# Optimization experiments

Hardware: AMD Instinct MI355X
Metric: run time of the kernel (lower is better)

The kernel has to match this reference:

```python
import jax, jax.numpy as jnp
import numpy as np

NETS = 32
NODES = [256, 512, 512, 128]
BATCH = 4096


def setup_inputs() -> dict:
    key = jax.random.key(0)
    ks = jax.random.split(key, 7)
    def lin_init(k, n_out, n_in):
        # mimic nn.Linear default init scale
        bound = 1.0 / np.sqrt(n_in)
        kw, kb = jax.random.split(k)
        W = jax.random.uniform(kw, (NETS, n_out, n_in), jnp.float32, -bound, bound)
        b = jax.random.uniform(kb, (NETS, n_out), jnp.float32, -bound, bound)
        return W, b
    x = jax.random.normal(ks[0], (BATCH, NODES[0]), jnp.float32)
    W1, b1 = lin_init(ks[1], NODES[1], NODES[0])
    W2, b2 = lin_init(ks[2], NODES[2], NODES[1])
    W3, b3 = lin_init(ks[3], NODES[3], NODES[2])
    return {"x": x, "W1": W1, "b1": b1, "W2": W2, "b2": b2, "W3": W3, "b3": b3}


def reference(x, W1, b1, W2, b2, W3, b3):
    # Ensemble of independent MLPs expressed as batched GEMMs over the `nets` axis.
    # x: [B, in]; Wl: [N, out_l, in_l]; bl: [N, out_l]
    h = jax.nn.relu(jnp.einsum('bi,noi->bno', x, W1) + b1)        # [B, N, 512]
    h = jax.nn.relu(jnp.einsum('bni,noi->bno', h, W2) + b2)       # [B, N, 512]
    out = jnp.einsum('bni,noi->bno', h, W3) + b3                  # [B, N, 128] (identity act)
    B = x.shape[0]
    # Concatenate per-net outputs along feature dim: y[:, n*out_len:(n+1)*out_len]
    return out.reshape(B, -1)
```

## Files before the change

### kernel.cpp

```cpp
#include <hip/hip_runtime.h>

#define NETS 32
#define BATCH 4096
#define D0 256
#define D1 512
#define D2 512
#define D3 128
#define MT 64
#define LDA (D0 + 8)
#define LDH (D1 + 8)

using half8 = __attribute__((ext_vector_type(8))) _Float16;
using half4 = __attribute__((ext_vector_type(4))) _Float16;
using f32x4 = __attribute__((ext_vector_type(4))) float;

#define W1_N (NETS * D1 * D0)
#define W2_N (NETS * D2 * D1)
#define W3_N (NETS * D3 * D2)

__global__ void cvt_weights(const float* __restrict__ W1, const float* __restrict__ W2,
                            const float* __restrict__ W3,
                            _Float16* __restrict__ W1h, _Float16* __restrict__ W2h,
                            _Float16* __restrict__ W3h) {
    const int i = blockIdx.x * blockDim.x + threadIdx.x;
    constexpr int T1 = W1_N / 8, T2 = W2_N / 8, T3 = W3_N / 8;
    const float* src;
    _Float16* dst;
    if (i < T1) {
        int u = i, l = u & 63, f = u >> 6;
        int kkni = f & 63, netw = f >> 6;
        int ni = kkni & 7, kk = kkni >> 3;
        int net = netw >> 2, w = netw & 3;
        int n = w * 128 + ni * 16 + (l & 15);
        int k = kk * 32 + (l >> 4) * 8;
        src = W1 + (size_t)net * D1 * D0 + (size_t)n * D0 + k;
        dst = W1h + (size_t)f * 512 + l * 8;
    } else if (i < T1 + T2) {
        int u = i - T1, l = u & 63, f = u >> 6;
        int kkni = f & 127, netw = f >> 7;
        int ni = kkni & 7, kk = kkni >> 3;
        int net = netw >> 2, w = netw & 3;
        int n = w * 128 + ni * 16 + (l & 15);
        int k = kk * 32 + (l >> 4) * 8;
        src = W2 + (size_t)net * D2 * D1 + (size_t)n * D1 + k;
        dst = W2h + (size_t)f * 512 + l * 8;
    } else {
        int u = i - T1 - T2, l = u & 63, f = u >> 6;
        int kkni = f & 31, netw = f >> 5;
        int ni = kkni & 1, kk = kkni >> 1;
        int net = netw >> 2, w = netw & 3;
        int n = w * 32 + ni * 16 + (l & 15);
        int k = kk * 32 + (l >> 4) * 8;
        src = W3 + (size_t)net * D3 * D2 + (size_t)n * D2 + k;
        dst = W3h + (size_t)f * 512 + l * 8;
    }
    float4 v0 = *reinterpret_cast<const float4*>(src);
    float4 v1 = *reinterpret_cast<const float4*>(src + 4);
    half8 o;
    o[0] = (_Float16)v0.x; o[1] = (_Float16)v0.y; o[2] = (_Float16)v0.z; o[3] = (_Float16)v0.w;
    o[4] = (_Float16)v1.x; o[5] = (_Float16)v1.y; o[6] = (_Float16)v1.z; o[7] = (_Float16)v1.w;
    *reinterpret_cast<half8*>(dst) = o;
}

template<int K, int NI, int G, int MI>
__device__ __forceinline__ void layer_mfma(const _Float16* As, int lda,
                                           const _Float16* __restrict__ wl,
                                           int lane16, int quad,
                                           f32x4 (&acc)[MI][NI]) {
    constexpr int NFR = (K / 32) * NI;
    constexpr int STEPS = NFR / G;
    half8 bcur[G], bnxt[G];
    half8 a[MI];
#pragma unroll
    for (int g = 0; g < G; ++g)
        bcur[g] = *reinterpret_cast<const half8*>(wl + (size_t)g * 512);
#pragma unroll
    for (int s = 0; s < STEPS; ++s) {
        const int fb = s * G;
        if (s + 1 < STEPS) {
#pragma unroll
            for (int g = 0; g < G; ++g)
                bnxt[g] = *reinterpret_cast<const half8*>(wl + (size_t)(fb + G + g) * 512);
        }
        if (fb % NI == 0) {
            const int kk = fb / NI;
#pragma unroll
            for (int mi = 0; mi < MI; ++mi)
                a[mi] = *reinterpret_cast<const half8*>(
                    As + (mi * 16 + lane16) * lda + kk * 32 + quad * 8);
        }
#pragma unroll
        for (int g = 0; g < G; ++g) {
            const int ni = (fb + g) % NI;
#pragma unroll
            for (int mi = 0; mi < MI; ++mi)
                acc[mi][ni] = __builtin_amdgcn_mfma_f32_16x16x32_f16(a[mi], bcur[g], acc[mi][ni], 0, 0, 0);
        }
        if (s + 1 < STEPS) {
#pragma unroll
            for (int g = 0; g < G; ++g) bcur[g] = bnxt[g];
        }
    }
}

template<int MI, int NI>
__device__ __forceinline__ void store_act(f32x4 (&acc)[MI][NI], const float* __restrict__ bias,
                                          _Float16* dst, int ldd, int n_base,
                                          int lane16, int quad) {
#pragma unroll
    for (int ni = 0; ni < NI; ++ni) {
        float bv = bias[n_base + ni * 16 + lane16];
        int col = n_base + ni * 16 + lane16;
#pragma unroll
        for (int mi = 0; mi < MI; ++mi) {
#pragma unroll
            for (int r = 0; r < 4; ++r) {
                float v = acc[mi][ni][r] + bv;
                v = fmaxf(v, 0.0f);
                int row = mi * 16 + quad * 4 + r;
                dst[row * ldd + col] = (_Float16)v;
            }
        }
    }
}

__global__ __launch_bounds__(256, 2) void mlp_fused(
    const float* __restrict__ X,
    const _Float16* __restrict__ W1h, const float* __restrict__ b1,
    const _Float16* __restrict__ W2h, const float* __restrict__ b2,
    const _Float16* __restrict__ W3h, const float* __restrict__ b3,
    float* __restrict__ out) {
    __shared__ __align__(16) _Float16 buf[MT * LDH];

    const int tid = threadIdx.x;
    const int w = tid >> 6;
    const int l = tid & 63;
    const int lane16 = l & 15;
    const int quad = l >> 4;

    const int bb = blockIdx.x;
    const int xcd = bb & 7;
    const int s = bb >> 3;
    const int net = xcd * 4 + (s >> 6);
    const int mt = s & 63;
    const int m0 = mt * MT;

    {
        const float* xsrc = X + (size_t)m0 * D0;
#pragma unroll
        for (int it = 0; it < 16; ++it) {
            int chunk = it * 256 + tid;
            int row = chunk >> 6;
            int c4 = chunk & 63;
            float4 v = *reinterpret_cast<const float4*>(xsrc + row * D0 + c4 * 4);
            half4 o;
            o[0] = (_Float16)v.x; o[1] = (_Float16)v.y;
            o[2] = (_Float16)v.z; o[3] = (_Float16)v.w;
            *reinterpret_cast<half4*>(&buf[row * LDA + c4 * 4]) = o;
        }
    }
    __syncthreads();

    {
        f32x4 acc[4][8] = {};
        const _Float16* wl = W1h + ((size_t)(net * 4 + w) * 64) * 512 + l * 8;
        layer_mfma<D0, 8, 4, 4>(buf, LDA, wl, lane16, quad, acc);
        __syncthreads();
        store_act<4, 8>(acc, b1 + net * D1, buf, LDH, w * 128, lane16, quad);
    }
    __syncthreads();

    {
        f32x4 acc[4][8] = {};
        const _Float16* wl = W2h + ((size_t)(net * 4 + w) * 128) * 512 + l * 8;
        layer_mfma<D1, 8, 4, 4>(buf, LDH, wl, lane16, quad, acc);
        __syncthreads();
        store_act<4, 8>(acc, b2 + net * D2, buf, LDH, w * 128, lane16, quad);
    }
    __syncthreads();

    {
        f32x4 acc[4][2] = {};
        const _Float16* wl = W3h + ((size_t)(net * 4 + w) * 32) * 512 + l * 8;
        layer_mfma<D2, 2, 2, 4>(buf, LDH, wl, lane16, quad, acc);
        const int n_base = w * 32;
#pragma unroll
        for (int ni = 0; ni < 2; ++ni) {
            float bv = b3[net * D3 + n_base + ni * 16 + lane16];
            int col = net * D3 + n_base + ni * 16 + lane16;
#pragma unroll
            for (int mi = 0; mi < 4; ++mi) {
#pragma unroll
                for (int r = 0; r < 4; ++r) {
                    int row = m0 + mi * 16 + quad * 4 + r;
                    out[(size_t)row * (NETS * D3) + col] = acc[mi][ni][r] + bv;
                }
            }
        }
    }
}

extern "C" void kernel_launch(void* const* d_in, const int* in_sizes, int n_in,
                              void* d_out, int out_size, void* d_ws, size_t ws_size,
                              hipStream_t stream) {
    const float* x  = (const float*)d_in[0];
    const float* W1 = (const float*)d_in[1];
    const float* b1 = (const float*)d_in[2];
    const float* W2 = (const float*)d_in[3];
    const float* b2 = (const float*)d_in[4];
    const float* W3 = (const float*)d_in[5];
    const float* b3 = (const float*)d_in[6];
    float* out = (float*)d_out;

    _Float16* W1h = (_Float16*)d_ws;
    _Float16* W2h = W1h + (size_t)W1_N;
    _Float16* W3h = W2h + (size_t)W2_N;

    const int totalT = (W1_N + W2_N + W3_N) / 8;
    cvt_weights<<<totalT / 256, 256, 0, stream>>>(W1, W2, W3, W1h, W2h, W3h);

    mlp_fused<<<NETS * (BATCH / MT), 256, 0, stream>>>(x, W1h, b1, W2h, b2, W3h, b3, out);
}
```

Before: 243.2 us.

## Deepen weight/activation prefetch ring and swap MFMA operands for vectorized epilogue

Replaces the single-stage weight double buffer with a DEPTH-deep register ring and adds an ADEPTH-deep prefetch of LDS activation fragments, to hide global and LDS latency behind MFMA work. It swaps the A/B operands of the MFMA so each lane holds four consecutive output columns. The bias-add/ReLU epilogue then writes half4 to LDS and float4 to global memory instead of scalar stores. The deeper ring raises VGPR pressure, which may threaten the 2-blocks-per-SM launch bound or cause spills.

```diff
diff --git a/kernel.cpp b/kernel.cpp
--- a/kernel.cpp
+++ b/kernel.cpp
@@ -62,43 +62,57 @@
     *reinterpret_cast<half8*>(dst) = o;
 }
 
-template<int K, int NI, int G, int MI>
+template<int K, int NI, int G, int MI, int DEPTH, int ADEPTH>
 __device__ __forceinline__ void layer_mfma(const _Float16* As, int lda,
                                            const _Float16* __restrict__ wl,
                                            int lane16, int quad,
                                            f32x4 (&acc)[MI][NI]) {
-    constexpr int NFR = (K / 32) * NI;
+    constexpr int KK = K / 32;
+    constexpr int NFR = KK * NI;
     constexpr int STEPS = NFR / G;
-    half8 bcur[G], bnxt[G];
-    half8 a[MI];
-#pragma unroll
-    for (int g = 0; g < G; ++g)
-        bcur[g] = *reinterpret_cast<const half8*>(wl + (size_t)g * 512);
+    static_assert(STEPS >= DEPTH, "prefetch ring deeper than steps");
+    half8 b[DEPTH][G];
+    half8 a[ADEPTH][MI];
+#pragma unroll
+    for (int d = 0; d < DEPTH; ++d)
+#pragma unroll
+        for (int g = 0; g < G; ++g)
+            b[d][g] = *reinterpret_cast<const half8*>(wl + (size_t)(d * G + g) * 512);
+#pragma unroll
+    for (int j = 0; j < ADEPTH - 1; ++j)
+#pragma unroll
+        for (int mi = 0; mi < MI; ++mi)
+            a[j][mi] = *reinterpret_cast<const half8*>(
+                As + (mi * 16 + lane16) * lda + j * 32 + quad * 8);
 #pragma unroll
     for (int s = 0; s < STEPS; ++s) {
+        const int cur = s % DEPTH;
         const int fb = s * G;
-        if (s + 1 < STEPS) {
-#pragma unroll
-            for (int g = 0; g < G; ++g)
-                bnxt[g] = *reinterpret_cast<const half8*>(wl + (size_t)(fb + G + g) * 512);
-        }
         if (fb % NI == 0) {
             const int kk = fb / NI;
+            const int pk = kk + ADEPTH - 1;
+            if (pk < KK) {
+#pragma unroll
+                for (int mi = 0; mi < MI; ++mi)
+                    a[pk % ADEPTH][mi] = *reinterpret_cast<const half8*>(
+                        As + (mi * 16 + lane16) * lda + pk * 32 + quad * 8);
+            }
+        }
+#pragma unroll
+        for (int g = 0; g < G; ++g) {
+            const int f = fb + g;
+            const int ni = f % NI;
+            const int ka = (f / NI) % ADEPTH;
 #pragma unroll
             for (int mi = 0; mi < MI; ++mi)
-                a[mi] = *reinterpret_cast<const half8*>(
-                    As + (mi * 16 + lane16) * lda + kk * 32 + quad * 8);
-        }
-#pragma unroll
-        for (int g = 0; g < G; ++g) {
-            const int ni = (fb + g) % NI;
-#pragma unroll
-            for (int mi = 0; mi < MI; ++mi)
-                acc[mi][ni] = __builtin_amdgcn_mfma_f32_16x16x32_f16(a[mi], bcur[g], acc[mi][ni], 0, 0, 0);
-        }
-        if (s + 1 < STEPS) {
-#pragma unroll
-            for (int g = 0; g < G; ++g) bcur[g] = bnxt[g];
+                acc[mi][ni] = __builtin_amdgcn_mfma_f32_16x16x32_f16(
+                    b[cur][g], a[ka][mi], acc[mi][ni], 0, 0, 0);
+        }
+        if (s + DEPTH < STEPS) {
+#pragma unroll
+            for (int g = 0; g < G; ++g)
+                b[cur][g] = *reinterpret_cast<const half8*>(
+                    wl + (size_t)((s + DEPTH) * G + g) * 512);
         }
     }
 }
@@ -109,17 +123,16 @@
                                           int lane16, int quad) {
 #pragma unroll
     for (int ni = 0; ni < NI; ++ni) {
-        float bv = bias[n_base + ni * 16 + lane16];
-        int col = n_base + ni * 16 + lane16;
+        const int n0 = n_base + ni * 16 + quad * 4;
+        const float4 bv = *reinterpret_cast<const float4*>(bias + n0);
 #pragma unroll
         for (int mi = 0; mi < MI; ++mi) {
-#pragma unroll
-            for (int r = 0; r < 4; ++r) {
-                float v = acc[mi][ni][r] + bv;
-                v = fmaxf(v, 0.0f);
-                int row = mi * 16 + quad * 4 + r;
-                dst[row * ldd + col] = (_Float16)v;
-            }
+            half4 o;
+            o[0] = (_Float16)fmaxf(acc[mi][ni][0] + bv.x, 0.0f);
+            o[1] = (_Float16)fmaxf(acc[mi][ni][1] + bv.y, 0.0f);
+            o[2] = (_Float16)fmaxf(acc[mi][ni][2] + bv.z, 0.0f);
+            o[3] = (_Float16)fmaxf(acc[mi][ni][3] + bv.w, 0.0f);
+            *reinterpret_cast<half4*>(&dst[(mi * 16 + lane16) * ldd + n0]) = o;
         }
     }
 }
@@ -164,7 +177,7 @@
     {
         f32x4 acc[4][8] = {};
         const _Float16* wl = W1h + ((size_t)(net * 4 + w) * 64) * 512 + l * 8;
-        layer_mfma<D0, 8, 4, 4>(buf, LDA, wl, lane16, quad, acc);
+        layer_mfma<D0, 8, 4, 4, 4, 2>(buf, LDA, wl, lane16, quad, acc);
         __syncthreads();
         store_act<4, 8>(acc, b1 + net * D1, buf, LDH, w * 128, lane16, quad);
     }
@@ -173,7 +186,7 @@
     {
         f32x4 acc[4][8] = {};
         const _Float16* wl = W2h + ((size_t)(net * 4 + w) * 128) * 512 + l * 8;
-        layer_mfma<D1, 8, 4, 4>(buf, LDH, wl, lane16, quad, acc);
+        layer_mfma<D1, 8, 4, 4, 4, 2>(buf, LDH, wl, lane16, quad, acc);
         __syncthreads();
         store_act<4, 8>(acc, b2 + net * D2, buf, LDH, w * 128, lane16, quad);
     }
@@ -182,19 +195,22 @@
     {
         f32x4 acc[4][2] = {};
         const _Float16* wl = W3h + ((size_t)(net * 4 + w) * 32) * 512 + l * 8;
-        layer_mfma<D2, 2, 2, 4>(buf, LDH, wl, lane16, quad, acc);
+        layer_mfma<D2, 2, 2, 4, 6, 4>(buf, LDH, wl, lane16, quad, acc);
         const int n_base = w * 32;
 #pragma unroll
         for (int ni = 0; ni < 2; ++ni) {
-            float bv = b3[net * D3 + n_base + ni * 16 + lane16];
-            int col = net * D3 + n_base + ni * 16 + lane16;
+            const int n0 = n_base + ni * 16 + quad * 4;
+            const float4 bv = *reinterpret_cast<const float4*>(b3 + net * D3 + n0);
 #pragma unroll
             for (int mi = 0; mi < 4; ++mi) {
-#pragma unroll
-                for (int r = 0; r < 4; ++r) {
-                    int row = m0 + mi * 16 + quad * 4 + r;
-                    out[(size_t)row * (NETS * D3) + col] = acc[mi][ni][r] + bv;
-                }
+                const int row = m0 + mi * 16 + lane16;
+                float4 v;
+                v.x = acc[mi][ni][0] + bv.x;
+                v.y = acc[mi][ni][1] + bv.y;
+                v.z = acc[mi][ni][2] + bv.z;
+                v.w = acc[mi][ni][3] + bv.w;
+                *reinterpret_cast<float4*>(
+                    &out[(size_t)row * (NETS * D3) + net * D3 + n0]) = v;
             }
         }
     }
```

Result: slower. 269.1 us (+10.6%).

## Use 8 waves per block and reorganize weight fragment layout with coalesced reads

Applied to the files above, without the earlier changes.

Doubles the block to 512 threads (8 waves), so each wave computes half as many output columns per layer and needs fewer accumulator registers. The launch bounds now ask for 4 blocks per CU to raise occupancy and hide weight-load latency. The weight conversion kernel is re-laid out to match the 8-wave split and now assigns lanes so adjacent threads read contiguous k, improving read coalescing, with a lane permutation on the store. The trade-off is more waves contending for LDS and barriers, and fewer MFMAs per A-fragment load, which lowers register-level reuse.

```diff
diff --git a/kernel.cpp b/kernel.cpp
--- a/kernel.cpp
+++ b/kernel.cpp
@@ -25,41 +25,43 @@
     const int i = blockIdx.x * blockDim.x + threadIdx.x;
     constexpr int T1 = W1_N / 8, T2 = W2_N / 8, T3 = W3_N / 8;
     const float* src;
-    _Float16* dst;
+    _Float16* dstf;
+    int l;
     if (i < T1) {
-        int u = i, l = u & 63, f = u >> 6;
-        int kkni = f & 63, netw = f >> 6;
-        int ni = kkni & 7, kk = kkni >> 3;
-        int net = netw >> 2, w = netw & 3;
-        int n = w * 128 + ni * 16 + (l & 15);
-        int k = kk * 32 + (l >> 4) * 8;
+        int u = i; l = u & 63; int f = u >> 6;
+        int ni = f & 3, kk = (f >> 2) & 7;
+        int netw = f >> 5;
+        int w = netw & 7, net = netw >> 3;
+        int n = w * 64 + ni * 16 + (l >> 2);
+        int k = kk * 32 + (l & 3) * 8;
         src = W1 + (size_t)net * D1 * D0 + (size_t)n * D0 + k;
-        dst = W1h + (size_t)f * 512 + l * 8;
+        dstf = W1h + (size_t)f * 512;
     } else if (i < T1 + T2) {
-        int u = i - T1, l = u & 63, f = u >> 6;
-        int kkni = f & 127, netw = f >> 7;
-        int ni = kkni & 7, kk = kkni >> 3;
-        int net = netw >> 2, w = netw & 3;
-        int n = w * 128 + ni * 16 + (l & 15);
-        int k = kk * 32 + (l >> 4) * 8;
+        int u = i - T1; l = u & 63; int f = u >> 6;
+        int ni = f & 3, kk = (f >> 2) & 15;
+        int netw = f >> 6;
+        int w = netw & 7, net = netw >> 3;
+        int n = w * 64 + ni * 16 + (l >> 2);
+        int k = kk * 32 + (l & 3) * 8;
         src = W2 + (size_t)net * D2 * D1 + (size_t)n * D1 + k;
-        dst = W2h + (size_t)f * 512 + l * 8;
+        dstf = W2h + (size_t)f * 512;
     } else {
-        int u = i - T1 - T2, l = u & 63, f = u >> 6;
-        int kkni = f & 31, netw = f >> 5;
-        int ni = kkni & 1, kk = kkni >> 1;
-        int net = netw >> 2, w = netw & 3;
-        int n = w * 32 + ni * 16 + (l & 15);
-        int k = kk * 32 + (l >> 4) * 8;
+        int u = i - T1 - T2; l = u & 63; int f = u >> 6;
+        int kk = f & 15;
+        int netw = f >> 4;
+        int w = netw & 7, net = netw >> 3;
+        int n = w * 16 + (l >> 2);
+        int k = kk * 32 + (l & 3) * 8;
         src = W3 + (size_t)net * D3 * D2 + (size_t)n * D2 + k;
-        dst = W3h + (size_t)f * 512 + l * 8;
+        dstf = W3h + (size_t)f * 512;
     }
     float4 v0 = *reinterpret_cast<const float4*>(src);
     float4 v1 = *reinterpret_cast<const float4*>(src + 4);
     half8 o;
     o[0] = (_Float16)v0.x; o[1] = (_Float16)v0.y; o[2] = (_Float16)v0.z; o[3] = (_Float16)v0.w;
     o[4] = (_Float16)v1.x; o[5] = (_Float16)v1.y; o[6] = (_Float16)v1.z; o[7] = (_Float16)v1.w;
-    *reinterpret_cast<half8*>(dst) = o;
+    const int lp = ((l & 3) << 4) | (l >> 2);
+    *reinterpret_cast<half8*>(dstf + lp * 8) = o;
 }
 
 template<int K, int NI, int G, int MI>
@@ -124,7 +126,7 @@
     }
 }
 
-__global__ __launch_bounds__(256, 2) void mlp_fused(
+__global__ __launch_bounds__(512, 4) void mlp_fused(
     const float* __restrict__ X,
     const _Float16* __restrict__ W1h, const float* __restrict__ b1,
     const _Float16* __restrict__ W2h, const float* __restrict__ b2,
@@ -148,8 +150,8 @@
     {
         const float* xsrc = X + (size_t)m0 * D0;
 #pragma unroll
-        for (int it = 0; it < 16; ++it) {
-            int chunk = it * 256 + tid;
+        for (int it = 0; it < 8; ++it) {
+            int chunk = it * 512 + tid;
             int row = chunk >> 6;
             int c4 = chunk & 63;
             float4 v = *reinterpret_cast<const float4*>(xsrc + row * D0 + c4 * 4);
@@ -162,39 +164,36 @@
     __syncthreads();
 
     {
-        f32x4 acc[4][8] = {};
-        const _Float16* wl = W1h + ((size_t)(net * 4 + w) * 64) * 512 + l * 8;
-        layer_mfma<D0, 8, 4, 4>(buf, LDA, wl, lane16, quad, acc);
+        f32x4 acc[4][4] = {};
+        const _Float16* wl = W1h + ((size_t)(net * 8 + w) * 32) * 512 + l * 8;
+        layer_mfma<D0, 4, 2, 4>(buf, LDA, wl, lane16, quad, acc);
         __syncthreads();
-        store_act<4, 8>(acc, b1 + net * D1, buf, LDH, w * 128, lane16, quad);
+        store_act<4, 4>(acc, b1 + net * D1, buf, LDH, w * 64, lane16, quad);
     }
     __syncthreads();
 
     {
-        f32x4 acc[4][8] = {};
-        const _Float16* wl = W2h + ((size_t)(net * 4 + w) * 128) * 512 + l * 8;
-        layer_mfma<D1, 8, 4, 4>(buf, LDH, wl, lane16, quad, acc);
+        f32x4 acc[4][4] = {};
+        const _Float16* wl = W2h + ((size_t)(net * 8 + w) * 64) * 512 + l * 8;
+        layer_mfma<D1, 4, 2, 4>(buf, LDH, wl, lane16, quad, acc);
         __syncthreads();
-        store_act<4, 8>(acc, b2 + net * D2, buf, LDH, w * 128, lane16, quad);
+        store_act<4, 4>(acc, b2 + net * D2, buf, LDH, w * 64, lane16, quad);
     }
     __syncthreads();
 
     {
-        f32x4 acc[4][2] = {};
-        const _Float16* wl = W3h + ((size_t)(net * 4 + w) * 32) * 512 + l * 8;
-        layer_mfma<D2, 2, 2, 4>(buf, LDH, wl, lane16, quad, acc);
-        const int n_base = w * 32;
-#pragma unroll
-        for (int ni = 0; ni < 2; ++ni) {
-            float bv = b3[net * D3 + n_base + ni * 16 + lane16];
-            int col = net * D3 + n_base + ni * 16 + lane16;
-#pragma unroll
-            for (int mi = 0; mi < 4; ++mi) {
-#pragma unroll
-                for (int r = 0; r < 4; ++r) {
-                    int row = m0 + mi * 16 + quad * 4 + r;
-                    out[(size_t)row * (NETS * D3) + col] = acc[mi][ni][r] + bv;
-                }
+        f32x4 acc[4][1] = {};
+        const _Float16* wl = W3h + ((size_t)(net * 8 + w) * 16) * 512 + l * 8;
+        layer_mfma<D2, 1, 1, 4>(buf, LDH, wl, lane16, quad, acc);
+        const int n_base = w * 16;
+        float bv = b3[net * D3 + n_base + lane16];
+        int col = net * D3 + n_base + lane16;
+#pragma unroll
+        for (int mi = 0; mi < 4; ++mi) {
+#pragma unroll
+            for (int r = 0; r < 4; ++r) {
+                int row = m0 + mi * 16 + quad * 4 + r;
+                out[(size_t)row * (NETS * D3) + col] = acc[mi][0][r] + bv;
             }
         }
     }
@@ -219,5 +218,5 @@
     const int totalT = (W1_N + W2_N + W3_N) / 8;
     cvt_weights<<<totalT / 256, 256, 0, stream>>>(W1, W2, W3, W1h, W2h, W3h);
 
-    mlp_fused<<<NETS * (BATCH / MT), 256, 0, stream>>>(x, W1h, b1, W2h, b2, W3h, b3, out);
-}
+    mlp_fused<<<NETS * (BATCH / MT), 512, 0, stream>>>(x, W1h, b1, W2h, b2, W3h, b3, out);
+}
```

Measured after the change: 247.4 us. Within noise of the previous version (+1.7%).
